# Performance work log

Measured on AMD Instinct MI355X. Metric: run time of the kernel, lower is better.

The kernel has to match this reference:

```python
import jax, jax.numpy as jnp
import numpy as np

N_NODES = 50000
N_RAND_EDGES = 800000
IN_FEATS = 128
NUM_HEADS = 4
OUT_FEATS = 32
NEG_SLOPE = 0.2


def setup_inputs() -> dict:
    key = jax.random.key(0)
    k_feat, k_src, k_dst, k_w, k_al, k_ar, k_b = jax.random.split(key, 7)
    feat = jax.random.normal(k_feat, (N_NODES, IN_FEATS), dtype=jnp.float32)
    # random edges + self-loops so every node has in-degree >= 1 (DGL requirement)
    src_r = jax.random.randint(k_src, (N_RAND_EDGES,), 0, N_NODES)
    dst_r = jax.random.randint(k_dst, (N_RAND_EDGES,), 0, N_NODES)
    loops = jnp.arange(N_NODES, dtype=src_r.dtype)
    src = jnp.concatenate([src_r, loops]).astype(jnp.int64)
    dst = jnp.concatenate([dst_r, loops]).astype(jnp.int64)
    W = jax.random.normal(k_w, (NUM_HEADS * OUT_FEATS, IN_FEATS), dtype=jnp.float32) * 0.05
    attn_l = jax.random.normal(k_al, (1, NUM_HEADS, OUT_FEATS), dtype=jnp.float32) * 0.1
    attn_r = jax.random.normal(k_ar, (1, NUM_HEADS, OUT_FEATS), dtype=jnp.float32) * 0.1
    bias = jnp.zeros((NUM_HEADS * OUT_FEATS,), dtype=jnp.float32)
    return {"feat": feat, "src": src, "dst": dst, "W": W,
            "attn_l": attn_l, "attn_r": attn_r, "bias": bias}


def _gat_forward(feat, src, dst, W, attn_l, attn_r, bias):
    n = feat.shape[0]
    # shared projection: in homogeneous path feat_src2 = feat_dst2 = fc(h)
    ft = (feat @ W.T).reshape(n, NUM_HEADS, OUT_FEATS)       # [N,H,D]
    el = jnp.sum(ft * attn_l, axis=-1)                        # [N,H]
    er = jnp.sum(ft * attn_r, axis=-1)                        # [N,H]
    e = el[src] + er[dst]                                     # [E,H]
    e = jnp.where(e > 0, e, NEG_SLOPE * e)                    # leaky_relu
    # edge softmax per destination node (numerically stable)
    m = jax.ops.segment_max(e, dst, num_segments=n)           # [N,H]
    ex = jnp.exp(e - m[dst])
    s = jax.ops.segment_sum(ex, dst, num_segments=n)          # [N,H]
    a = ex / s[dst]                                           # [E,H]
    # u_mul_e -> sum : attention-weighted aggregation
    msg1 = ft[src] * a[:, :, None]                            # [E,H,D]
    initial_ft = jax.ops.segment_sum(msg1, dst, num_segments=n)
    # u_mul_v -> sum : elementwise src*dst product aggregation
    msg2 = ft[src] * ft[dst]                                  # [E,H,D]
    add_ft = jax.ops.segment_sum(msg2, dst, num_segments=n)
    rst = initial_ft + add_ft + bias.reshape(1, NUM_HEADS, OUT_FEATS)
    return rst


def reference(feat, src, dst, W, attn_l, attn_r, bias):
    return _gat_forward(feat, src, dst, W, attn_l, attn_r, bias)
```

## Files before the change

### kernel.cpp

```cpp
#include <hip/hip_runtime.h>
#include <hip/hip_bf16.h>

#define IN_FEATS 128
#define HD 128
#define NEG_SLOPE 0.2f
#define LDR 128
#define CAP 64
#define NBLK 256
#define BINW 256
#define CAPB 5120

typedef short s8v __attribute__((ext_vector_type(8)));
typedef float f4v __attribute__((ext_vector_type(4)));

static __device__ __forceinline__ unsigned short f2bf(float f) {
    unsigned int u = __float_as_uint(f);
    unsigned int r = (u + 0x7FFFu + ((u >> 16) & 1u)) >> 16;
    return (unsigned short)r;
}
static __device__ __forceinline__ float bf2f(unsigned short h) {
    return __uint_as_float(((unsigned int)h) << 16);
}


__global__ __launch_bounds__(256) void bin_count(const int* __restrict__ dst, int E,
                                                 int* __restrict__ cntBB, int nbins) {
    __shared__ int hist[256];
    hist[threadIdx.x] = 0;
    __syncthreads();
    const int chunk = (E + NBLK - 1) / NBLK;
    const int base = blockIdx.x * chunk;
    const int end = min(base + chunk, E);
    for (int i = base + threadIdx.x; i < end; i += 256)
        atomicAdd(&hist[dst[i] >> 8], 1);
    __syncthreads();
    if (threadIdx.x < nbins)
        cntBB[threadIdx.x * NBLK + blockIdx.x] = hist[threadIdx.x];
}

__global__ __launch_bounds__(64) void bin_scan(const int* __restrict__ cntBB,
                                               int* __restrict__ offBB,
                                               int* __restrict__ binTotal) {
    const int bin = blockIdx.x;
    const int lane = threadIdx.x;
    int base = 0;
    for (int c = 0; c < NBLK; c += 64) {
        int v = cntBB[bin * NBLK + c + lane];
        int x = v;
#pragma unroll
        for (int d = 1; d < 64; d <<= 1) {
            int t = __shfl_up(x, d);
            if (lane >= d) x += t;
        }
        offBB[bin * NBLK + c + lane] = base + x - v;
        base += __shfl(x, 63);
    }
    if (lane == 0) binTotal[bin] = base;
}

__global__ __launch_bounds__(256) void bin_scatter(const int* __restrict__ src,
                                                   const int* __restrict__ dst, int E,
                                                   const int* __restrict__ offBB,
                                                   unsigned int* __restrict__ binbuf,
                                                   int nbins) {
    __shared__ int obase[256];
    __shared__ int lcnt[256];
    lcnt[threadIdx.x] = 0;
    obase[threadIdx.x] = (threadIdx.x < nbins) ? offBB[threadIdx.x * NBLK + blockIdx.x] : 0;
    __syncthreads();
    const int chunk = (E + NBLK - 1) / NBLK;
    const int base = blockIdx.x * chunk;
    const int end = min(base + chunk, E);
    for (int i = base + threadIdx.x; i < end; i += 256) {
        int d = dst[i];
        int s = src[i];
        int bin = d >> 8;
        int r = atomicAdd(&lcnt[bin], 1);
        int idx = obase[bin] + r;
        if (idx < CAPB)
            binbuf[(size_t)bin * CAPB + idx] =
                ((unsigned int)(d & 255) << 16) | (unsigned int)s;
    }
}

__global__ __launch_bounds__(256) void bucket_build(const unsigned int* __restrict__ binbuf,
                                                    const int* __restrict__ binTotal,
                                                    int* __restrict__ cnt,
                                                    int* __restrict__ bucket, int N) {
    __shared__ int lcnt[256];
    lcnt[threadIdx.x] = 0;
    __syncthreads();
    const int bin = blockIdx.x;
    const int total = min(binTotal[bin], CAPB);
    const unsigned int* bb = binbuf + (size_t)bin * CAPB;
    for (int i = threadIdx.x; i < total; i += 256) {
        unsigned int v = bb[i];
        int dl = (int)(v >> 16);
        int s  = (int)(v & 0xFFFFu);
        int pos = atomicAdd(&lcnt[dl], 1);
        if (pos < CAP)
            bucket[(((size_t)(bin << 8) + dl) << 6) + pos] = s;
    }
    __syncthreads();
    int gn = (bin << 8) + threadIdx.x;
    if (gn < N) cnt[gn] = lcnt[threadIdx.x];
}

#define GM 64
#define LDA 136
__global__ __launch_bounds__(256) void gemm_kernel(const float* __restrict__ feat,
                                                   const float* __restrict__ W,
                                                   const float* __restrict__ attn_l,
                                                   const float* __restrict__ attn_r,
                                                   unsigned short* __restrict__ ftb,
                                                   float* __restrict__ el,
                                                   float* __restrict__ er, int N) {
    __shared__ unsigned short Wb[128][LDA];
    __shared__ unsigned short Ab[GM][LDA];

    const int tid   = threadIdx.x;
    const int wave  = tid >> 6;
    const int lane  = tid & 63;
    const int m     = lane & 15;
    const int quad  = lane >> 4;
    const int rbase = blockIdx.x * GM;

    const float4* W4 = (const float4*)W;
    for (int i = tid; i < 4096; i += 256) {
        int r = i >> 5, q = i & 31;
        float4 w = W4[i];
        ushort4 o;
        o.x = f2bf(w.x); o.y = f2bf(w.y); o.z = f2bf(w.z); o.w = f2bf(w.w);
        *(ushort4*)&Wb[r][q * 4] = o;
    }
    const float4* F4 = (const float4*)feat;
    for (int i = tid; i < 2048; i += 256) {
        int r = i >> 5, q = i & 31;
        int gr = rbase + r;
        float4 v = (gr < N) ? F4[(size_t)gr * 32 + q]
                            : make_float4(0.f, 0.f, 0.f, 0.f);
        ushort4 o;
        o.x = f2bf(v.x); o.y = f2bf(v.y); o.z = f2bf(v.z); o.w = f2bf(v.w);
        *(ushort4*)&Ab[r][q * 4] = o;
    }
    __syncthreads();

    f4v acc[8];
#pragma unroll
    for (int t = 0; t < 8; ++t) acc[t] = (f4v){0.f, 0.f, 0.f, 0.f};

    const int arow = wave * 16 + m;
#pragma unroll
    for (int k0 = 0; k0 < 4; ++k0) {
        s8v a = *(const s8v*)&Ab[arow][k0 * 32 + quad * 8];
#pragma unroll
        for (int t = 0; t < 8; ++t) {
            s8v b = *(const s8v*)&Wb[t * 16 + m][k0 * 32 + quad * 8];
            acc[t] = __builtin_amdgcn_mfma_f32_16x16x32_bf16(a, b, acc[t], 0, 0, 0);
        }
    }

#pragma unroll
    for (int reg = 0; reg < 4; ++reg) {
        int gr = rbase + wave * 16 + quad * 4 + reg;
        if (gr < N) {
            unsigned short* dstrow = &ftb[(size_t)gr * LDR];
#pragma unroll
            for (int t = 0; t < 8; ++t)
                dstrow[t * 16 + m] = f2bf(acc[t][reg]);
        }
    }

    float al[8], ar[8];
#pragma unroll
    for (int t = 0; t < 8; ++t) {
        al[t] = attn_l[t * 16 + m];
        ar[t] = attn_r[t * 16 + m];
    }
#pragma unroll
    for (int h = 0; h < 4; ++h) {
#pragma unroll
        for (int reg = 0; reg < 4; ++reg) {
            float pl = acc[2 * h][reg] * al[2 * h] + acc[2 * h + 1][reg] * al[2 * h + 1];
            float pr = acc[2 * h][reg] * ar[2 * h] + acc[2 * h + 1][reg] * ar[2 * h + 1];
            pl += __shfl_xor(pl, 1); pr += __shfl_xor(pr, 1);
            pl += __shfl_xor(pl, 2); pr += __shfl_xor(pr, 2);
            pl += __shfl_xor(pl, 4); pr += __shfl_xor(pr, 4);
            pl += __shfl_xor(pl, 8); pr += __shfl_xor(pr, 8);
            if (m == 0) {
                int gr = rbase + wave * 16 + quad * 4 + reg;
                if (gr < N) {
                    el[gr * 4 + h] = pl;
                    er[gr * 4 + h] = pr;
                }
            }
        }
    }
}

__global__ __launch_bounds__(256) void aggregate_kernel(
        const unsigned short* __restrict__ ftb, const float* __restrict__ el,
        const float* __restrict__ er, const int* __restrict__ cnt,
        const int* __restrict__ bucket, const float* __restrict__ bias,
        float* __restrict__ out, int N) {
    const int n    = (blockIdx.x * blockDim.x + threadIdx.x) >> 6;
    const int lane = threadIdx.x & 63;
    if (n >= N) return;
    const int h  = lane >> 4;
    const int c0 = lane * 2;

    const float ern = er[(n << 2) + h];
    ushort2 tn = *(const ushort2*)(ftb + (size_t)n * LDR + c0);
    const float ftn0 = bf2f(tn.x), ftn1 = bf2f(tn.y);

    int deg = min(cnt[n], CAP);
    const int* eb = bucket + ((size_t)n << 6);

    float a0 = 0.f, a1 = 0.f;
    float b0 = 0.f, b1 = 0.f;
    float sum = 0.f;

    int i = 0;
    for (; i + 4 <= deg; i += 4) {
        int sA = eb[i + 0], sB = eb[i + 1], sC = eb[i + 2], sD = eb[i + 3];
        float eA = el[(sA << 2) + h];
        float eB = el[(sB << 2) + h];
        float eC = el[(sC << 2) + h];
        float eD = el[(sD << 2) + h];
        ushort2 fA = *(const ushort2*)(ftb + (size_t)sA * LDR + c0);
        ushort2 fB = *(const ushort2*)(ftb + (size_t)sB * LDR + c0);
        ushort2 fC = *(const ushort2*)(ftb + (size_t)sC * LDR + c0);
        ushort2 fD = *(const ushort2*)(ftb + (size_t)sD * LDR + c0);
        eA += ern; eB += ern; eC += ern; eD += ern;
        eA = eA > 0.f ? eA : NEG_SLOPE * eA;
        eB = eB > 0.f ? eB : NEG_SLOPE * eB;
        eC = eC > 0.f ? eC : NEG_SLOPE * eC;
        eD = eD > 0.f ? eD : NEG_SLOPE * eD;
        float xA = __expf(eA), xB = __expf(eB);
        float xC = __expf(eC), xD = __expf(eD);
        float fAx = bf2f(fA.x), fAy = bf2f(fA.y);
        float fBx = bf2f(fB.x), fBy = bf2f(fB.y);
        float fCx = bf2f(fC.x), fCy = bf2f(fC.y);
        float fDx = bf2f(fD.x), fDy = bf2f(fD.y);
        sum += (xA + xB) + (xC + xD);
        a0 += xA * fAx + xB * fBx + xC * fCx + xD * fDx;
        a1 += xA * fAy + xB * fBy + xC * fCy + xD * fDy;
        b0 += (fAx + fBx) + (fCx + fDx);
        b1 += (fAy + fBy) + (fCy + fDy);
    }
    for (; i < deg; ++i) {
        int s = eb[i];
        float e = el[(s << 2) + h] + ern;
        e = e > 0.f ? e : NEG_SLOPE * e;
        float x = __expf(e);
        ushort2 f = *(const ushort2*)(ftb + (size_t)s * LDR + c0);
        float fx = bf2f(f.x), fy = bf2f(f.y);
        sum += x;
        a0 += x * fx; a1 += x * fy;
        b0 += fx;     b1 += fy;
    }

    float inv = 1.f / sum;
    float2 o;
    o.x = a0 * inv + ftn0 * b0 + bias[c0];
    o.y = a1 * inv + ftn1 * b1 + bias[c0 + 1];
    *(float2*)(out + (size_t)n * HD + c0) = o;
}

extern "C" void kernel_launch(void* const* d_in, const int* in_sizes, int n_in,
                              void* d_out, int out_size, void* d_ws, size_t ws_size,
                              hipStream_t stream) {
    const float* feat   = (const float*)d_in[0];
    const int*   src    = (const int*)d_in[1];
    const int*   dst    = (const int*)d_in[2];
    const float* W      = (const float*)d_in[3];
    const float* attn_l = (const float*)d_in[4];
    const float* attn_r = (const float*)d_in[5];
    const float* bias   = (const float*)d_in[6];

    const int N = in_sizes[0] / IN_FEATS;
    const int E = in_sizes[1];
    const int nbins = (N + BINW - 1) / BINW;

    char* p = (char*)d_ws;
    auto alloc = [&](size_t bytes) {
        char* q = p;
        p += (bytes + 255) & ~(size_t)255;
        return q;
    };
    unsigned short* ftb   = (unsigned short*)alloc((size_t)N * LDR * 2);
    float* el       = (float*)alloc((size_t)N * 4 * 4);
    float* er       = (float*)alloc((size_t)N * 4 * 4);
    int*   cnt      = (int*)alloc((size_t)N * 4);
    int*   bucket   = (int*)alloc((size_t)N * CAP * 4);
    unsigned int* binbuf = (unsigned int*)alloc((size_t)nbins * CAPB * 4);
    int*   cntBB    = (int*)alloc((size_t)nbins * NBLK * 4);
    int*   offBB    = (int*)alloc((size_t)nbins * NBLK * 4);
    int*   binTotal = (int*)alloc((size_t)nbins * 4);

    bin_count<<<NBLK, 256, 0, stream>>>(dst, E, cntBB, nbins);
    bin_scan<<<nbins, 64, 0, stream>>>(cntBB, offBB, binTotal);
    bin_scatter<<<NBLK, 256, 0, stream>>>(src, dst, E, offBB, binbuf, nbins);
    bucket_build<<<nbins, 256, 0, stream>>>(binbuf, binTotal, cnt, bucket, N);

    const int gemm_blocks = (N + GM - 1) / GM;
    gemm_kernel<<<gemm_blocks, 256, 0, stream>>>(feat, W, attn_l, attn_r,
                                                 ftb, el, er, N);

    long long threads = (long long)N * 64;
    int agg_blocks = (int)((threads + 255) / 256);
    aggregate_kernel<<<agg_blocks, 256, 0, stream>>>(ftb, el, er, cnt, bucket,
                                                     bias, (float*)d_out, N);
}
```

Before: 181.7 us.

## Fuse graph bucketing and projection GEMM into one cooperative kernel

Merges the bin-count, scan, scatter, bucket-build and GEMM kernels into one cooperative kernel that uses grid-wide syncs. The GEMM blocks run alongside the histogram blocks, and the counting grid is widened to 368 blocks. This is meant to remove four launch gaps and to overlap the projection with edge bucketing. The aggregation loop is also unrolled by 8 with batched index and feature loads and a wave-uniform node index, to get more gathers in flight. The cost is three grid barriers and an occupancy requirement of 3 blocks per CU; if the cooperative launch fails, the code falls back to the old separate kernels.

```diff
diff --git a/kernel.cpp b/kernel.cpp
--- a/kernel.cpp
+++ b/kernel.cpp
@@ -1,14 +1,24 @@
 #include <hip/hip_runtime.h>
 #include <hip/hip_bf16.h>
+#include <hip/hip_cooperative_groups.h>
+
+namespace cg = cooperative_groups;
 
 #define IN_FEATS 128
 #define HD 128
 #define NEG_SLOPE 0.2f
 #define LDR 128
 #define CAP 64
-#define NBLK 256
 #define BINW 256
 #define CAPB 5120
+#define NBLK 256
+
+#define CB    368
+#define GEMMB 400
+#define GRID_ALL (CB + GEMMB)
+
+#define GM 64
+#define LDA 136
 
 typedef short s8v __attribute__((ext_vector_type(8)));
 typedef float f4v __attribute__((ext_vector_type(4)));
@@ -22,117 +32,17 @@
     return __uint_as_float(((unsigned int)h) << 16);
 }
 
-
-__global__ __launch_bounds__(256) void bin_count(const int* __restrict__ dst, int E,
-                                                 int* __restrict__ cntBB, int nbins) {
-    __shared__ int hist[256];
-    hist[threadIdx.x] = 0;
-    __syncthreads();
-    const int chunk = (E + NBLK - 1) / NBLK;
-    const int base = blockIdx.x * chunk;
-    const int end = min(base + chunk, E);
-    for (int i = base + threadIdx.x; i < end; i += 256)
-        atomicAdd(&hist[dst[i] >> 8], 1);
-    __syncthreads();
-    if (threadIdx.x < nbins)
-        cntBB[threadIdx.x * NBLK + blockIdx.x] = hist[threadIdx.x];
-}
-
-__global__ __launch_bounds__(64) void bin_scan(const int* __restrict__ cntBB,
-                                               int* __restrict__ offBB,
-                                               int* __restrict__ binTotal) {
-    const int bin = blockIdx.x;
-    const int lane = threadIdx.x;
-    int base = 0;
-    for (int c = 0; c < NBLK; c += 64) {
-        int v = cntBB[bin * NBLK + c + lane];
-        int x = v;
-#pragma unroll
-        for (int d = 1; d < 64; d <<= 1) {
-            int t = __shfl_up(x, d);
-            if (lane >= d) x += t;
-        }
-        offBB[bin * NBLK + c + lane] = base + x - v;
-        base += __shfl(x, 63);
-    }
-    if (lane == 0) binTotal[bin] = base;
-}
-
-__global__ __launch_bounds__(256) void bin_scatter(const int* __restrict__ src,
-                                                   const int* __restrict__ dst, int E,
-                                                   const int* __restrict__ offBB,
-                                                   unsigned int* __restrict__ binbuf,
-                                                   int nbins) {
-    __shared__ int obase[256];
-    __shared__ int lcnt[256];
-    lcnt[threadIdx.x] = 0;
-    obase[threadIdx.x] = (threadIdx.x < nbins) ? offBB[threadIdx.x * NBLK + blockIdx.x] : 0;
-    __syncthreads();
-    const int chunk = (E + NBLK - 1) / NBLK;
-    const int base = blockIdx.x * chunk;
-    const int end = min(base + chunk, E);
-    for (int i = base + threadIdx.x; i < end; i += 256) {
-        int d = dst[i];
-        int s = src[i];
-        int bin = d >> 8;
-        int r = atomicAdd(&lcnt[bin], 1);
-        int idx = obase[bin] + r;
-        if (idx < CAPB)
-            binbuf[(size_t)bin * CAPB + idx] =
-                ((unsigned int)(d & 255) << 16) | (unsigned int)s;
-    }
-}
-
-__global__ __launch_bounds__(256) void bucket_build(const unsigned int* __restrict__ binbuf,
-                                                    const int* __restrict__ binTotal,
-                                                    int* __restrict__ cnt,
-                                                    int* __restrict__ bucket, int N) {
-    __shared__ int lcnt[256];
-    lcnt[threadIdx.x] = 0;
-    __syncthreads();
-    const int bin = blockIdx.x;
-    const int total = min(binTotal[bin], CAPB);
-    const unsigned int* bb = binbuf + (size_t)bin * CAPB;
-    for (int i = threadIdx.x; i < total; i += 256) {
-        unsigned int v = bb[i];
-        int dl = (int)(v >> 16);
-        int s  = (int)(v & 0xFFFFu);
-        int pos = atomicAdd(&lcnt[dl], 1);
-        if (pos < CAP)
-            bucket[(((size_t)(bin << 8) + dl) << 6) + pos] = s;
-    }
-    __syncthreads();
-    int gn = (bin << 8) + threadIdx.x;
-    if (gn < N) cnt[gn] = lcnt[threadIdx.x];
-}
-
-#define GM 64
-#define LDA 136
-__global__ __launch_bounds__(256) void gemm_kernel(const float* __restrict__ feat,
-                                                   const float* __restrict__ W,
-                                                   const float* __restrict__ attn_l,
-                                                   const float* __restrict__ attn_r,
-                                                   unsigned short* __restrict__ ftb,
-                                                   float* __restrict__ el,
-                                                   float* __restrict__ er, int N) {
-    __shared__ unsigned short Wb[128][LDA];
-    __shared__ unsigned short Ab[GM][LDA];
-
-    const int tid   = threadIdx.x;
-    const int wave  = tid >> 6;
-    const int lane  = tid & 63;
-    const int m     = lane & 15;
-    const int quad  = lane >> 4;
-    const int rbase = blockIdx.x * GM;
-
-    const float4* W4 = (const float4*)W;
-    for (int i = tid; i < 4096; i += 256) {
-        int r = i >> 5, q = i & 31;
-        float4 w = W4[i];
-        ushort4 o;
-        o.x = f2bf(w.x); o.y = f2bf(w.y); o.z = f2bf(w.z); o.w = f2bf(w.w);
-        *(ushort4*)&Wb[r][q * 4] = o;
-    }
+static __device__ __forceinline__ void gemm_tile(
+        unsigned short (*Wb)[LDA], unsigned short (*Ab)[LDA],
+        const float* __restrict__ feat, const float* __restrict__ attn_l,
+        const float* __restrict__ attn_r, unsigned short* __restrict__ ftb,
+        float* __restrict__ el, float* __restrict__ er, int N, int rbase) {
+    const int tid  = threadIdx.x;
+    const int wave = tid >> 6;
+    const int lane = tid & 63;
+    const int m    = lane & 15;
+    const int quad = lane >> 4;
+
     const float4* F4 = (const float4*)feat;
     for (int i = tid; i < 2048; i += 256) {
         int r = i >> 5, q = i & 31;
@@ -198,22 +108,232 @@
     }
 }
 
+static __device__ __forceinline__ void stage_W(unsigned short (*Wb)[LDA],
+                                               const float* __restrict__ W) {
+    const float4* W4 = (const float4*)W;
+    for (int i = threadIdx.x; i < 4096; i += 256) {
+        int r = i >> 5, q = i & 31;
+        float4 w = W4[i];
+        ushort4 o;
+        o.x = f2bf(w.x); o.y = f2bf(w.y); o.z = f2bf(w.z); o.w = f2bf(w.w);
+        *(ushort4*)&Wb[r][q * 4] = o;
+    }
+}
+
+__global__ __launch_bounds__(256, 3) void build_all(
+        const float* __restrict__ feat, const float* __restrict__ W,
+        const float* __restrict__ attn_l, const float* __restrict__ attn_r,
+        const int* __restrict__ src, const int* __restrict__ dst, int E,
+        int* __restrict__ cntBB, int* __restrict__ offBB,
+        int* __restrict__ binTotal, unsigned int* __restrict__ binbuf,
+        int* __restrict__ cnt, int* __restrict__ bucket,
+        unsigned short* __restrict__ ftb, float* __restrict__ el,
+        float* __restrict__ er, int N, int nbins) {
+    __shared__ __align__(16) char smem[52224];
+    const int tid = threadIdx.x;
+    const int bid = blockIdx.x;
+    cg::grid_group grid = cg::this_grid();
+
+    if (bid < CB) {
+        int* hist = (int*)smem;
+        hist[tid] = 0;
+        __syncthreads();
+        const int chunk = (E + CB - 1) / CB;
+        const int base = bid * chunk;
+        const int end = min(base + chunk, E);
+        for (int i = base + tid; i < end; i += 256)
+            atomicAdd(&hist[dst[i] >> 8], 1);
+        __syncthreads();
+        if (tid < nbins) cntBB[tid * CB + bid] = hist[tid];
+    } else {
+        unsigned short (*Wb)[LDA] = (unsigned short (*)[LDA])smem;
+        unsigned short (*Ab)[LDA] = (unsigned short (*)[LDA])(smem + 128 * LDA * 2);
+        stage_W(Wb, W);
+        const int ntiles = (N + GM - 1) / GM;
+        for (int t = bid - CB; t < ntiles; t += GEMMB) {
+            __syncthreads();
+            gemm_tile(Wb, Ab, feat, attn_l, attn_r, ftb, el, er, N, t * GM);
+        }
+    }
+    grid.sync();
+
+    if (bid < nbins && tid < 64) {
+        const int bin = bid;
+        const int lane = tid;
+        int base = 0;
+        for (int c = 0; c < CB; c += 64) {
+            int idx = c + lane;
+            int v = (idx < CB) ? cntBB[bin * CB + idx] : 0;
+            int x = v;
+#pragma unroll
+            for (int d = 1; d < 64; d <<= 1) {
+                int t = __shfl_up(x, d);
+                if (lane >= d) x += t;
+            }
+            if (idx < CB) offBB[bin * CB + idx] = base + x - v;
+            base += __shfl(x, 63);
+        }
+        if (lane == 0) binTotal[bin] = base;
+    }
+    grid.sync();
+
+    if (bid < CB) {
+        int* obase = (int*)smem;
+        int* lcnt  = ((int*)smem) + 256;
+        lcnt[tid] = 0;
+        obase[tid] = (tid < nbins) ? offBB[tid * CB + bid] : 0;
+        __syncthreads();
+        const int chunk = (E + CB - 1) / CB;
+        const int base = bid * chunk;
+        const int end = min(base + chunk, E);
+        for (int i = base + tid; i < end; i += 256) {
+            int d = dst[i];
+            int s = src[i];
+            int bin = d >> 8;
+            int r = atomicAdd(&lcnt[bin], 1);
+            int idx = obase[bin] + r;
+            if (idx < CAPB)
+                binbuf[(size_t)bin * CAPB + idx] =
+                    ((unsigned int)(d & 255) << 16) | (unsigned int)s;
+        }
+    }
+    grid.sync();
+
+    if (bid < nbins) {
+        int* lcnt = (int*)smem;
+        lcnt[tid] = 0;
+        __syncthreads();
+        const int bin = bid;
+        const int total = min(binTotal[bin], CAPB);
+        const unsigned int* bb = binbuf + (size_t)bin * CAPB;
+        for (int i = tid; i < total; i += 256) {
+            unsigned int v = bb[i];
+            int dl = (int)(v >> 16);
+            int s  = (int)(v & 0xFFFFu);
+            int pos = atomicAdd(&lcnt[dl], 1);
+            if (pos < CAP)
+                bucket[(((size_t)(bin << 8) + dl) << 6) + pos] = s;
+        }
+        __syncthreads();
+        int gn = (bin << 8) + tid;
+        if (gn < N) cnt[gn] = lcnt[tid];
+    }
+}
+
+__global__ __launch_bounds__(256) void bin_count(const int* __restrict__ dst, int E,
+                                                 int* __restrict__ cntBB, int nbins) {
+    __shared__ int hist[256];
+    hist[threadIdx.x] = 0;
+    __syncthreads();
+    const int chunk = (E + NBLK - 1) / NBLK;
+    const int base = blockIdx.x * chunk;
+    const int end = min(base + chunk, E);
+    for (int i = base + threadIdx.x; i < end; i += 256)
+        atomicAdd(&hist[dst[i] >> 8], 1);
+    __syncthreads();
+    if (threadIdx.x < nbins)
+        cntBB[threadIdx.x * NBLK + blockIdx.x] = hist[threadIdx.x];
+}
+
+__global__ __launch_bounds__(64) void bin_scan(const int* __restrict__ cntBB,
+                                               int* __restrict__ offBB,
+                                               int* __restrict__ binTotal) {
+    const int bin = blockIdx.x;
+    const int lane = threadIdx.x;
+    int base = 0;
+    for (int c = 0; c < NBLK; c += 64) {
+        int v = cntBB[bin * NBLK + c + lane];
+        int x = v;
+#pragma unroll
+        for (int d = 1; d < 64; d <<= 1) {
+            int t = __shfl_up(x, d);
+            if (lane >= d) x += t;
+        }
+        offBB[bin * NBLK + c + lane] = base + x - v;
+        base += __shfl(x, 63);
+    }
+    if (lane == 0) binTotal[bin] = base;
+}
+
+__global__ __launch_bounds__(256) void bin_scatter(const int* __restrict__ src,
+                                                   const int* __restrict__ dst, int E,
+                                                   const int* __restrict__ offBB,
+                                                   unsigned int* __restrict__ binbuf,
+                                                   int nbins) {
+    __shared__ int obase[256];
+    __shared__ int lcnt[256];
+    lcnt[threadIdx.x] = 0;
+    obase[threadIdx.x] = (threadIdx.x < nbins) ? offBB[threadIdx.x * NBLK + blockIdx.x] : 0;
+    __syncthreads();
+    const int chunk = (E + NBLK - 1) / NBLK;
+    const int base = blockIdx.x * chunk;
+    const int end = min(base + chunk, E);
+    for (int i = base + threadIdx.x; i < end; i += 256) {
+        int d = dst[i];
+        int s = src[i];
+        int bin = d >> 8;
+        int r = atomicAdd(&lcnt[bin], 1);
+        int idx = obase[bin] + r;
+        if (idx < CAPB)
+            binbuf[(size_t)bin * CAPB + idx] =
+                ((unsigned int)(d & 255) << 16) | (unsigned int)s;
+    }
+}
+
+__global__ __launch_bounds__(256) void bucket_build(const unsigned int* __restrict__ binbuf,
+                                                    const int* __restrict__ binTotal,
+                                                    int* __restrict__ cnt,
+                                                    int* __restrict__ bucket, int N) {
+    __shared__ int lcnt[256];
+    lcnt[threadIdx.x] = 0;
+    __syncthreads();
+    const int bin = blockIdx.x;
+    const int total = min(binTotal[bin], CAPB);
+    const unsigned int* bb = binbuf + (size_t)bin * CAPB;
+    for (int i = threadIdx.x; i < total; i += 256) {
+        unsigned int v = bb[i];
+        int dl = (int)(v >> 16);
+        int s  = (int)(v & 0xFFFFu);
+        int pos = atomicAdd(&lcnt[dl], 1);
+        if (pos < CAP)
+            bucket[(((size_t)(bin << 8) + dl) << 6) + pos] = s;
+    }
+    __syncthreads();
+    int gn = (bin << 8) + threadIdx.x;
+    if (gn < N) cnt[gn] = lcnt[threadIdx.x];
+}
+
+__global__ __launch_bounds__(256) void gemm_kernel(const float* __restrict__ feat,
+                                                   const float* __restrict__ W,
+                                                   const float* __restrict__ attn_l,
+                                                   const float* __restrict__ attn_r,
+                                                   unsigned short* __restrict__ ftb,
+                                                   float* __restrict__ el,
+                                                   float* __restrict__ er, int N) {
+    __shared__ unsigned short Wb[128][LDA];
+    __shared__ unsigned short Ab[GM][LDA];
+    stage_W(Wb, W);
+    __syncthreads();
+    gemm_tile(Wb, Ab, feat, attn_l, attn_r, ftb, el, er, N, blockIdx.x * GM);
+}
+
 __global__ __launch_bounds__(256) void aggregate_kernel(
         const unsigned short* __restrict__ ftb, const float* __restrict__ el,
         const float* __restrict__ er, const int* __restrict__ cnt,
         const int* __restrict__ bucket, const float* __restrict__ bias,
         float* __restrict__ out, int N) {
-    const int n    = (blockIdx.x * blockDim.x + threadIdx.x) >> 6;
+    int n = (blockIdx.x * blockDim.x + threadIdx.x) >> 6;
+    if (n >= N) return;
+    n = __builtin_amdgcn_readfirstlane(n);
     const int lane = threadIdx.x & 63;
-    if (n >= N) return;
     const int h  = lane >> 4;
     const int c0 = lane * 2;
 
     const float ern = er[(n << 2) + h];
-    ushort2 tn = *(const ushort2*)(ftb + (size_t)n * LDR + c0);
+    ushort2 tn = *(const ushort2*)(ftb + ((size_t)n << 7) + c0);
     const float ftn0 = bf2f(tn.x), ftn1 = bf2f(tn.y);
 
-    int deg = min(cnt[n], CAP);
+    const int deg = min(cnt[n], CAP);
     const int* eb = bucket + ((size_t)n << 6);
 
     float a0 = 0.f, a1 = 0.f;
@@ -221,43 +341,56 @@
     float sum = 0.f;
 
     int i = 0;
+    for (; i + 8 <= deg; i += 8) {
+        int sx[8];
+#pragma unroll
+        for (int j = 0; j < 8; ++j) sx[j] = eb[i + j];
+        float ev[8]; unsigned int fv[8];
+#pragma unroll
+        for (int j = 0; j < 8; ++j) {
+            ev[j] = el[(sx[j] << 2) + h];
+            fv[j] = *(const unsigned int*)(ftb + ((size_t)sx[j] << 7) + c0);
+        }
+#pragma unroll
+        for (int j = 0; j < 8; ++j) {
+            float e = ev[j] + ern;
+            e = e > 0.f ? e : NEG_SLOPE * e;
+            float x = __expf(e);
+            float f0 = __uint_as_float(fv[j] << 16);
+            float f1 = __uint_as_float(fv[j] & 0xFFFF0000u);
+            sum += x;
+            a0 += x * f0; a1 += x * f1;
+            b0 += f0;     b1 += f1;
+        }
+    }
     for (; i + 4 <= deg; i += 4) {
-        int sA = eb[i + 0], sB = eb[i + 1], sC = eb[i + 2], sD = eb[i + 3];
-        float eA = el[(sA << 2) + h];
-        float eB = el[(sB << 2) + h];
-        float eC = el[(sC << 2) + h];
-        float eD = el[(sD << 2) + h];
-        ushort2 fA = *(const ushort2*)(ftb + (size_t)sA * LDR + c0);
-        ushort2 fB = *(const ushort2*)(ftb + (size_t)sB * LDR + c0);
-        ushort2 fC = *(const ushort2*)(ftb + (size_t)sC * LDR + c0);
-        ushort2 fD = *(const ushort2*)(ftb + (size_t)sD * LDR + c0);
-        eA += ern; eB += ern; eC += ern; eD += ern;
-        eA = eA > 0.f ? eA : NEG_SLOPE * eA;
-        eB = eB > 0.f ? eB : NEG_SLOPE * eB;
-        eC = eC > 0.f ? eC : NEG_SLOPE * eC;
-        eD = eD > 0.f ? eD : NEG_SLOPE * eD;
-        float xA = __expf(eA), xB = __expf(eB);
-        float xC = __expf(eC), xD = __expf(eD);
-        float fAx = bf2f(fA.x), fAy = bf2f(fA.y);
-        float fBx = bf2f(fB.x), fBy = bf2f(fB.y);
-        float fCx = bf2f(fC.x), fCy = bf2f(fC.y);
-        float fDx = bf2f(fD.x), fDy = bf2f(fD.y);
-        sum += (xA + xB) + (xC + xD);
-        a0 += xA * fAx + xB * fBx + xC * fCx + xD * fDx;
-        a1 += xA * fAy + xB * fBy + xC * fCy + xD * fDy;
-        b0 += (fAx + fBx) + (fCx + fDx);
-        b1 += (fAy + fBy) + (fCy + fDy);
+        int sx[4];
+#pragma unroll
+        for (int j = 0; j < 4; ++j) sx[j] = eb[i + j];
+#pragma unroll
+        for (int j = 0; j < 4; ++j) {
+            float e = el[(sx[j] << 2) + h] + ern;
+            unsigned int f = *(const unsigned int*)(ftb + ((size_t)sx[j] << 7) + c0);
+            e = e > 0.f ? e : NEG_SLOPE * e;
+            float x = __expf(e);
+            float f0 = __uint_as_float(f << 16);
+            float f1 = __uint_as_float(f & 0xFFFF0000u);
+            sum += x;
+            a0 += x * f0; a1 += x * f1;
+            b0 += f0;     b1 += f1;
+        }
     }
     for (; i < deg; ++i) {
         int s = eb[i];
         float e = el[(s << 2) + h] + ern;
         e = e > 0.f ? e : NEG_SLOPE * e;
         float x = __expf(e);
-        ushort2 f = *(const ushort2*)(ftb + (size_t)s * LDR + c0);
-        float fx = bf2f(f.x), fy = bf2f(f.y);
+        unsigned int f = *(const unsigned int*)(ftb + ((size_t)s << 7) + c0);
+        float f0 = __uint_as_float(f << 16);
+        float f1 = __uint_as_float(f & 0xFFFF0000u);
         sum += x;
-        a0 += x * fx; a1 += x * fy;
-        b0 += fx;     b1 += fy;
+        a0 += x * f0; a1 += x * f1;
+        b0 += f0;     b1 += f1;
     }
 
     float inv = 1.f / sum;
@@ -294,18 +427,31 @@
     int*   cnt      = (int*)alloc((size_t)N * 4);
     int*   bucket   = (int*)alloc((size_t)N * CAP * 4);
     unsigned int* binbuf = (unsigned int*)alloc((size_t)nbins * CAPB * 4);
-    int*   cntBB    = (int*)alloc((size_t)nbins * NBLK * 4);
-    int*   offBB    = (int*)alloc((size_t)nbins * NBLK * 4);
+    int*   cntBB    = (int*)alloc((size_t)nbins * CB * 4);
+    int*   offBB    = (int*)alloc((size_t)nbins * CB * 4);
     int*   binTotal = (int*)alloc((size_t)nbins * 4);
 
-    bin_count<<<NBLK, 256, 0, stream>>>(dst, E, cntBB, nbins);
-    bin_scan<<<nbins, 64, 0, stream>>>(cntBB, offBB, binTotal);
-    bin_scatter<<<NBLK, 256, 0, stream>>>(src, dst, E, offBB, binbuf, nbins);
-    bucket_build<<<nbins, 256, 0, stream>>>(binbuf, binTotal, cnt, bucket, N);
-
-    const int gemm_blocks = (N + GM - 1) / GM;
-    gemm_kernel<<<gemm_blocks, 256, 0, stream>>>(feat, W, attn_l, attn_r,
-                                                 ftb, el, er, N);
+    {
+        int E_ = E, N_ = N, nbins_ = nbins;
+        void* args[] = {
+            (void*)&feat, (void*)&W, (void*)&attn_l, (void*)&attn_r,
+            (void*)&src, (void*)&dst, (void*)&E_,
+            (void*)&cntBB, (void*)&offBB, (void*)&binTotal, (void*)&binbuf,
+            (void*)&cnt, (void*)&bucket, (void*)&ftb, (void*)&el, (void*)&er,
+            (void*)&N_, (void*)&nbins_
+        };
+        hipError_t err = hipLaunchCooperativeKernel(
+            (const void*)build_all, dim3(GRID_ALL), dim3(256), args, 0, stream);
+        if (err != hipSuccess) {
+            bin_count<<<NBLK, 256, 0, stream>>>(dst, E, cntBB, nbins);
+            bin_scan<<<nbins, 64, 0, stream>>>(cntBB, offBB, binTotal);
+            bin_scatter<<<NBLK, 256, 0, stream>>>(src, dst, E, offBB, binbuf, nbins);
+            bucket_build<<<nbins, 256, 0, stream>>>(binbuf, binTotal, cnt, bucket, N);
+            const int gemm_blocks = (N + GM - 1) / GM;
+            gemm_kernel<<<gemm_blocks, 256, 0, stream>>>(feat, W, attn_l, attn_r,
+                                                         ftb, el, er, N);
+        }
+    }
 
     long long threads = (long long)N * 64;
     int agg_blocks = (int)((threads + 255) / 256);
```

Measured after the change: 451.2 us. 2.48x slower.

## Fuse bin counting into GEMM launch and fold scan into scatter and build

Applied to the files above, without the earlier changes.

Merges the edge histogram and the projection GEMM into a single launch, with the first NBLK blocks doing counting and the rest doing GEMM tiles. The separate scan kernel is removed. Scatter blocks now compute their prefix offsets by summing earlier blocks' counts serially, and bucket_build reduces per-bin totals itself. This cuts two launches and lets the histogram overlap with the GEMM. In exchange, the scatter kernel does redundant serial prefix work of up to 255 loads per thread, and the count blocks reserve the large shared allocation.

```diff
diff --git a/kernel.cpp b/kernel.cpp
--- a/kernel.cpp
+++ b/kernel.cpp
@@ -6,9 +6,11 @@
 #define NEG_SLOPE 0.2f
 #define LDR 128
 #define CAP 64
-#define NBLK 256
 #define BINW 256
 #define CAPB 5120
+#define NBLK 256
+#define GM 64
+#define LDA 136
 
 typedef short s8v __attribute__((ext_vector_type(8)));
 typedef float f4v __attribute__((ext_vector_type(4)));
@@ -22,117 +24,29 @@
     return __uint_as_float(((unsigned int)h) << 16);
 }
 
-
-__global__ __launch_bounds__(256) void bin_count(const int* __restrict__ dst, int E,
-                                                 int* __restrict__ cntBB, int nbins) {
-    __shared__ int hist[256];
-    hist[threadIdx.x] = 0;
-    __syncthreads();
-    const int chunk = (E + NBLK - 1) / NBLK;
-    const int base = blockIdx.x * chunk;
-    const int end = min(base + chunk, E);
-    for (int i = base + threadIdx.x; i < end; i += 256)
-        atomicAdd(&hist[dst[i] >> 8], 1);
-    __syncthreads();
-    if (threadIdx.x < nbins)
-        cntBB[threadIdx.x * NBLK + blockIdx.x] = hist[threadIdx.x];
-}
-
-__global__ __launch_bounds__(64) void bin_scan(const int* __restrict__ cntBB,
-                                               int* __restrict__ offBB,
-                                               int* __restrict__ binTotal) {
-    const int bin = blockIdx.x;
-    const int lane = threadIdx.x;
-    int base = 0;
-    for (int c = 0; c < NBLK; c += 64) {
-        int v = cntBB[bin * NBLK + c + lane];
-        int x = v;
-#pragma unroll
-        for (int d = 1; d < 64; d <<= 1) {
-            int t = __shfl_up(x, d);
-            if (lane >= d) x += t;
-        }
-        offBB[bin * NBLK + c + lane] = base + x - v;
-        base += __shfl(x, 63);
-    }
-    if (lane == 0) binTotal[bin] = base;
-}
-
-__global__ __launch_bounds__(256) void bin_scatter(const int* __restrict__ src,
-                                                   const int* __restrict__ dst, int E,
-                                                   const int* __restrict__ offBB,
-                                                   unsigned int* __restrict__ binbuf,
-                                                   int nbins) {
-    __shared__ int obase[256];
-    __shared__ int lcnt[256];
-    lcnt[threadIdx.x] = 0;
-    obase[threadIdx.x] = (threadIdx.x < nbins) ? offBB[threadIdx.x * NBLK + blockIdx.x] : 0;
-    __syncthreads();
-    const int chunk = (E + NBLK - 1) / NBLK;
-    const int base = blockIdx.x * chunk;
-    const int end = min(base + chunk, E);
-    for (int i = base + threadIdx.x; i < end; i += 256) {
-        int d = dst[i];
-        int s = src[i];
-        int bin = d >> 8;
-        int r = atomicAdd(&lcnt[bin], 1);
-        int idx = obase[bin] + r;
-        if (idx < CAPB)
-            binbuf[(size_t)bin * CAPB + idx] =
-                ((unsigned int)(d & 255) << 16) | (unsigned int)s;
-    }
-}
-
-__global__ __launch_bounds__(256) void bucket_build(const unsigned int* __restrict__ binbuf,
-                                                    const int* __restrict__ binTotal,
-                                                    int* __restrict__ cnt,
-                                                    int* __restrict__ bucket, int N) {
-    __shared__ int lcnt[256];
-    lcnt[threadIdx.x] = 0;
-    __syncthreads();
-    const int bin = blockIdx.x;
-    const int total = min(binTotal[bin], CAPB);
-    const unsigned int* bb = binbuf + (size_t)bin * CAPB;
-    for (int i = threadIdx.x; i < total; i += 256) {
-        unsigned int v = bb[i];
-        int dl = (int)(v >> 16);
-        int s  = (int)(v & 0xFFFFu);
-        int pos = atomicAdd(&lcnt[dl], 1);
-        if (pos < CAP)
-            bucket[(((size_t)(bin << 8) + dl) << 6) + pos] = s;
-    }
-    __syncthreads();
-    int gn = (bin << 8) + threadIdx.x;
-    if (gn < N) cnt[gn] = lcnt[threadIdx.x];
-}
-
-#define GM 64
-#define LDA 136
-__global__ __launch_bounds__(256) void gemm_kernel(const float* __restrict__ feat,
-                                                   const float* __restrict__ W,
-                                                   const float* __restrict__ attn_l,
-                                                   const float* __restrict__ attn_r,
-                                                   unsigned short* __restrict__ ftb,
-                                                   float* __restrict__ el,
-                                                   float* __restrict__ er, int N) {
-    __shared__ unsigned short Wb[128][LDA];
-    __shared__ unsigned short Ab[GM][LDA];
-
-    const int tid   = threadIdx.x;
-    const int wave  = tid >> 6;
-    const int lane  = tid & 63;
-    const int m     = lane & 15;
-    const int quad  = lane >> 4;
-    const int rbase = blockIdx.x * GM;
-
+static __device__ __forceinline__ void stage_W(unsigned short (*Wb)[LDA],
+                                               const float* __restrict__ W) {
     const float4* W4 = (const float4*)W;
-    for (int i = tid; i < 4096; i += 256) {
+    for (int i = threadIdx.x; i < 4096; i += 256) {
         int r = i >> 5, q = i & 31;
         float4 w = W4[i];
         ushort4 o;
         o.x = f2bf(w.x); o.y = f2bf(w.y); o.z = f2bf(w.z); o.w = f2bf(w.w);
         *(ushort4*)&Wb[r][q * 4] = o;
     }
+}
+
+static __device__ __forceinline__ void gemm_tile(
+        unsigned short (*Wb)[LDA], unsigned short (*Ab)[LDA],
+        const float* __restrict__ feat, const float* __restrict__ attn_l,
+        const float* __restrict__ attn_r, unsigned short* __restrict__ ftb,
+        float* __restrict__ el, float* __restrict__ er, int N, int rbase) {
+    const int tid  = threadIdx.x;
+    const int wave = tid >> 6;
+    const int lane = tid & 63;
+    const int m    = lane & 15;
+    const int quad = lane >> 4;
+
     const float4* F4 = (const float4*)feat;
     for (int i = tid; i < 2048; i += 256) {
         int r = i >> 5, q = i & 31;
@@ -196,6 +110,92 @@
             }
         }
     }
+}
+
+__global__ __launch_bounds__(256) void count_gemm(
+        const float* __restrict__ feat, const float* __restrict__ W,
+        const float* __restrict__ attn_l, const float* __restrict__ attn_r,
+        const int* __restrict__ dst, int E, int* __restrict__ cntBB,
+        unsigned short* __restrict__ ftb, float* __restrict__ el,
+        float* __restrict__ er, int N, int nbins) {
+    __shared__ __align__(16) char smem[52224];
+    const int tid = threadIdx.x;
+    if (blockIdx.x < NBLK) {
+        int* hist = (int*)smem;
+        hist[tid] = 0;
+        __syncthreads();
+        const int chunk = (E + NBLK - 1) / NBLK;
+        const int base = blockIdx.x * chunk;
+        const int end = min(base + chunk, E);
+        for (int i = base + tid; i < end; i += 256)
+            atomicAdd(&hist[dst[i] >> 8], 1);
+        __syncthreads();
+        cntBB[blockIdx.x * 256 + tid] = hist[tid];
+        return;
+    }
+    unsigned short (*Wb)[LDA] = (unsigned short (*)[LDA])smem;
+    unsigned short (*Ab)[LDA] = (unsigned short (*)[LDA])(smem + 128 * LDA * 2);
+    stage_W(Wb, W);
+    gemm_tile(Wb, Ab, feat, attn_l, attn_r, ftb, el, er, N,
+              (blockIdx.x - NBLK) * GM);
+}
+
+__global__ __launch_bounds__(256) void scan_scatter(
+        const int* __restrict__ src, const int* __restrict__ dst, int E,
+        const int* __restrict__ cntBB, unsigned int* __restrict__ binbuf,
+        int nbins) {
+    __shared__ int obase[256];
+    __shared__ int lcnt[256];
+    const int tid = threadIdx.x;
+    const int bid = blockIdx.x;
+    int ob = 0;
+    for (int b = 0; b < bid; ++b)
+        ob += cntBB[b * 256 + tid];
+    obase[tid] = ob;
+    lcnt[tid] = 0;
+    __syncthreads();
+    const int chunk = (E + NBLK - 1) / NBLK;
+    const int base = bid * chunk;
+    const int end = min(base + chunk, E);
+    for (int i = base + tid; i < end; i += 256) {
+        int d = dst[i];
+        int s = src[i];
+        int bin = d >> 8;
+        int r = atomicAdd(&lcnt[bin], 1);
+        int idx = obase[bin] + r;
+        if (idx < CAPB)
+            binbuf[(size_t)bin * CAPB + idx] =
+                ((unsigned int)(d & 255) << 16) | (unsigned int)s;
+    }
+}
+
+__global__ __launch_bounds__(256) void bucket_build(
+        const unsigned int* __restrict__ binbuf, const int* __restrict__ cntBB,
+        int* __restrict__ cnt, int* __restrict__ bucket, int N) {
+    __shared__ int lcnt[256];
+    __shared__ int red[256];
+    const int bin = blockIdx.x;
+    const int tid = threadIdx.x;
+    lcnt[tid] = 0;
+    red[tid] = cntBB[tid * 256 + bin];
+    __syncthreads();
+    for (int s = 128; s > 0; s >>= 1) {
+        if (tid < s) red[tid] += red[tid + s];
+        __syncthreads();
+    }
+    const int total = min(red[0], CAPB);
+    const unsigned int* bb = binbuf + (size_t)bin * CAPB;
+    for (int i = tid; i < total; i += 256) {
+        unsigned int v = bb[i];
+        int dl = (int)(v >> 16);
+        int s  = (int)(v & 0xFFFFu);
+        int pos = atomicAdd(&lcnt[dl], 1);
+        if (pos < CAP)
+            bucket[(((size_t)(bin << 8) + dl) << 6) + pos] = s;
+    }
+    __syncthreads();
+    int gn = (bin << 8) + tid;
+    if (gn < N) cnt[gn] = lcnt[tid];
 }
 
 __global__ __launch_bounds__(256) void aggregate_kernel(
@@ -294,18 +294,15 @@
     int*   cnt      = (int*)alloc((size_t)N * 4);
     int*   bucket   = (int*)alloc((size_t)N * CAP * 4);
     unsigned int* binbuf = (unsigned int*)alloc((size_t)nbins * CAPB * 4);
-    int*   cntBB    = (int*)alloc((size_t)nbins * NBLK * 4);
-    int*   offBB    = (int*)alloc((size_t)nbins * NBLK * 4);
-    int*   binTotal = (int*)alloc((size_t)nbins * 4);
-
-    bin_count<<<NBLK, 256, 0, stream>>>(dst, E, cntBB, nbins);
-    bin_scan<<<nbins, 64, 0, stream>>>(cntBB, offBB, binTotal);
-    bin_scatter<<<NBLK, 256, 0, stream>>>(src, dst, E, offBB, binbuf, nbins);
-    bucket_build<<<nbins, 256, 0, stream>>>(binbuf, binTotal, cnt, bucket, N);
+    int*   cntBB    = (int*)alloc((size_t)NBLK * 256 * 4);
 
     const int gemm_blocks = (N + GM - 1) / GM;
-    gemm_kernel<<<gemm_blocks, 256, 0, stream>>>(feat, W, attn_l, attn_r,
-                                                 ftb, el, er, N);
+    count_gemm<<<NBLK + gemm_blocks, 256, 0, stream>>>(
+        feat, W, attn_l, attn_r, dst, E, cntBB, ftb, el, er, N, nbins);
+
+    scan_scatter<<<NBLK, 256, 0, stream>>>(src, dst, E, cntBB, binbuf, nbins);
+
+    bucket_build<<<nbins, 256, 0, stream>>>(binbuf, cntBB, cnt, bucket, N);
 
     long long threads = (long long)N * 64;
     int agg_blocks = (int)((threads + 255) / 256);
```

Result: slower. 200.6 us (+10.4%).
